# Kernel optimization log

Hardware: AMD Instinct MI355X
Metric: run time of the kernel (lower is better)

The kernel has to match this reference:

```python
import jax, jax.numpy as jnp
import numpy as np

B, V, L = 256, 128000, 2048
EPS = 1e-05


def setup_inputs() -> dict:
    key = jax.random.key(0)
    k1, k2, k3, k4, k5 = jax.random.split(key, 5)
    logits_next = jax.random.normal(k1, (B, V), jnp.float32)
    token_ids = jax.random.randint(k2, (B, L), 0, V, jnp.int32)
    presence_penalties = jax.random.uniform(k3, (B,), jnp.float32) * 1.5
    temperatures = jax.random.uniform(k4, (B,), jnp.float32, 0.5, 1.5)
    # make first quarter of the batch greedy (temperature == 0)
    temperatures = temperatures.at[: B // 4].set(0.0)
    u = jax.random.uniform(k5, (B, V), jnp.float32, 1e-9, 1.0)
    gumbel = -jnp.log(-jnp.log(u))  # Gumbel(0,1) noise for multinomial sampling
    return {
        "logits_next": logits_next,
        "token_ids": token_ids,
        "presence_penalties": presence_penalties,
        "temperatures": temperatures,
        "gumbel": gumbel,
    }


def reference(logits_next, token_ids, presence_penalties, temperatures, gumbel):
    Bn, Vn = logits_next.shape
    # presence mask: 1.0 where token id appeared in the history (counts > 0)
    rows = jnp.arange(Bn, dtype=jnp.int32)[:, None]  # [B,1]
    presence = jnp.zeros((Bn, Vn), logits_next.dtype).at[rows, token_ids].set(1.0)
    penalized = logits_next - presence_penalties[:, None] * presence

    greedy = temperatures < EPS  # [B]
    safe_t = jnp.where(greedy, jnp.float32(1.0), temperatures)
    scaled = penalized / safe_t[:, None]

    # greedy rows: plain argmax; sample rows: Gumbel-max == multinomial(softmax)
    greedy_tok = jnp.argmax(penalized, axis=-1)
    sampled_tok = jnp.argmax(scaled + gumbel, axis=-1)
    token_ids_next = jnp.where(greedy, greedy_tok, sampled_tok)
    return token_ids_next.astype(jnp.int32)
```

## Files before the change

kernel.cpp:

```cpp
#include <hip/hip_runtime.h>
#include <math.h>

#define BATCH 256
#define VOCAB 128000
#define HIST  2048
#define EPS_T 1e-5f

#define MASK_WORDS_ROW (VOCAB / 32)

#define ABLOCK 512

#define SEGS 25
#define SEG_ELEMS (VOCAB / SEGS)
#define SEG_VEC   (SEG_ELEMS / 4)
#define SEG_WORDS (SEG_ELEMS / 32)
#define BBLOCK 256
#define BWAVES (BBLOCK / 64)

__global__ __launch_bounds__(ABLOCK, 1) void mask_kernel(
    const int* __restrict__ token_ids,
    unsigned int* __restrict__ gmask)
{
    __shared__ unsigned int m[MASK_WORDS_ROW];
    const int b = blockIdx.x, tid = threadIdx.x;

    for (int i = tid; i < MASK_WORDS_ROW; i += ABLOCK) m[i] = 0u;
    __syncthreads();

    const int4* rt = (const int4*)(token_ids + (size_t)b * HIST);
    int4 t = rt[tid];
    atomicOr(&m[t.x >> 5], 1u << (t.x & 31));
    atomicOr(&m[t.y >> 5], 1u << (t.y & 31));
    atomicOr(&m[t.z >> 5], 1u << (t.z & 31));
    atomicOr(&m[t.w >> 5], 1u << (t.w & 31));
    __syncthreads();

    unsigned int* gr = gmask + (size_t)b * MASK_WORDS_ROW;
    for (int i = tid; i < MASK_WORDS_ROW; i += ABLOCK) gr[i] = m[i];
}

__device__ __forceinline__ void upd(float s, int idx, float& best, int& besti) {
    if (s > best || (s == best && idx < besti)) { best = s; besti = idx; }
}

__device__ __forceinline__ void body4(float4 l, unsigned w, int sh, float pen,
                                      int idx0, float& best, int& besti) {
    float e[4] = {l.x, l.y, l.z, l.w};
    #pragma unroll
    for (int j = 0; j < 4; j++) {
        float present = (float)((w >> (sh + j)) & 1u);
        float p = e[j] - pen * present;
        upd(p, idx0 + j, best, besti);
    }
}

__device__ __forceinline__ void body4s(float4 l, float4 g, unsigned w, int sh,
                                       float pen, float temp,
                                       int idx0, float& best, int& besti) {
    float e[4]  = {l.x, l.y, l.z, l.w};
    float gv[4] = {g.x, g.y, g.z, g.w};
    #pragma unroll
    for (int j = 0; j < 4; j++) {
        float present = (float)((w >> (sh + j)) & 1u);
        float p = e[j] - pen * present;
        float s = p / temp + gv[j];
        upd(s, idx0 + j, best, besti);
    }
}

__global__ __launch_bounds__(BBLOCK, 1) void scan_kernel(
    const float* __restrict__ logits,
    const float* __restrict__ gumbel,
    const unsigned int* __restrict__ gmask,
    const float* __restrict__ penalties,
    const float* __restrict__ temps,
    float* __restrict__ pvals,
    int*   __restrict__ pidxs)
{
    __shared__ float wval[BWAVES];
    __shared__ int   widx[BWAVES];

    const int blk = blockIdx.x;
    const int b   = blk / SEGS;
    const int seg = blk - b * SEGS;
    const int tid = threadIdx.x;

    const float pen    = penalties[b];
    const float temp   = temps[b];
    const bool  greedy = (temp < EPS_T);

    const float4*       lg = (const float4*)(logits + (size_t)b * VOCAB) + seg * SEG_VEC;
    const float4*       gm = (const float4*)(gumbel + (size_t)b * VOCAB) + seg * SEG_VEC;
    const unsigned int* mw = gmask + (size_t)b * MASK_WORDS_ROW + seg * SEG_WORDS;

    float best  = -INFINITY;
    int   besti = 0x7fffffff;
    const int sh    = (tid * 4) & 31;
    const int abs0  = seg * SEG_ELEMS + tid * 4;
    const int wbase = tid >> 3;

    if (greedy) {
        float4 l0 = lg[tid];
        float4 l1 = lg[tid + 1 * BBLOCK];
        float4 l2 = lg[tid + 2 * BBLOCK];
        float4 l3 = lg[tid + 3 * BBLOCK];
        float4 l4 = lg[tid + 4 * BBLOCK];
        unsigned w0 = mw[wbase];
        unsigned w1 = mw[wbase + 32];
        unsigned w2 = mw[wbase + 64];
        unsigned w3 = mw[wbase + 96];
        unsigned w4 = mw[wbase + 128];
        __builtin_amdgcn_sched_barrier(0);
        body4(l0, w0, sh, pen, abs0 + 0 * BBLOCK * 4, best, besti);
        body4(l1, w1, sh, pen, abs0 + 1 * BBLOCK * 4, best, besti);
        body4(l2, w2, sh, pen, abs0 + 2 * BBLOCK * 4, best, besti);
        body4(l3, w3, sh, pen, abs0 + 3 * BBLOCK * 4, best, besti);
        body4(l4, w4, sh, pen, abs0 + 4 * BBLOCK * 4, best, besti);
    } else {
        float4 l0 = lg[tid];
        float4 l1 = lg[tid + 1 * BBLOCK];
        float4 l2 = lg[tid + 2 * BBLOCK];
        float4 l3 = lg[tid + 3 * BBLOCK];
        float4 l4 = lg[tid + 4 * BBLOCK];
        float4 g0 = gm[tid];
        float4 g1 = gm[tid + 1 * BBLOCK];
        float4 g2 = gm[tid + 2 * BBLOCK];
        float4 g3 = gm[tid + 3 * BBLOCK];
        float4 g4 = gm[tid + 4 * BBLOCK];
        unsigned w0 = mw[wbase];
        unsigned w1 = mw[wbase + 32];
        unsigned w2 = mw[wbase + 64];
        unsigned w3 = mw[wbase + 96];
        unsigned w4 = mw[wbase + 128];
        __builtin_amdgcn_sched_barrier(0);
        body4s(l0, g0, w0, sh, pen, temp, abs0 + 0 * BBLOCK * 4, best, besti);
        body4s(l1, g1, w1, sh, pen, temp, abs0 + 1 * BBLOCK * 4, best, besti);
        body4s(l2, g2, w2, sh, pen, temp, abs0 + 2 * BBLOCK * 4, best, besti);
        body4s(l3, g3, w3, sh, pen, temp, abs0 + 3 * BBLOCK * 4, best, besti);
        body4s(l4, g4, w4, sh, pen, temp, abs0 + 4 * BBLOCK * 4, best, besti);
    }

    #pragma unroll
    for (int off = 32; off > 0; off >>= 1) {
        float ov = __shfl_down(best, off, 64);
        int   oi = __shfl_down(besti, off, 64);
        if (ov > best || (ov == best && oi < besti)) { best = ov; besti = oi; }
    }
    const int wave = tid >> 6, lane = tid & 63;
    if (lane == 0) { wval[wave] = best; widx[wave] = besti; }
    __syncthreads();

    if (tid == 0) {
        #pragma unroll
        for (int wv = 1; wv < BWAVES; wv++) {
            if (wval[wv] > best || (wval[wv] == best && widx[wv] < besti)) {
                best = wval[wv]; besti = widx[wv];
            }
        }
        pvals[seg * BATCH + b] = best;
        pidxs[seg * BATCH + b] = besti;
    }
}

__global__ void reduce_kernel(const float* __restrict__ pvals,
                              const int*   __restrict__ pidxs,
                              int*         __restrict__ out)
{
    const int b = threadIdx.x;
    float best  = pvals[b];
    int   besti = pidxs[b];
    #pragma unroll
    for (int s = 1; s < SEGS; s++) {
        float v = pvals[s * BATCH + b];
        if (v > best) { best = v; besti = pidxs[s * BATCH + b]; }
    }
    out[b] = besti;
}

extern "C" void kernel_launch(void* const* d_in, const int* in_sizes, int n_in,
                              void* d_out, int out_size, void* d_ws, size_t ws_size,
                              hipStream_t stream) {
    const float* logits    = (const float*)d_in[0];
    const int*   token_ids = (const int*)d_in[1];
    const float* penalties = (const float*)d_in[2];
    const float* temps     = (const float*)d_in[3];
    const float* gumbel    = (const float*)d_in[4];
    int* out = (int*)d_out;

    unsigned int* gmask = (unsigned int*)d_ws;
    float* pvals = (float*)((char*)d_ws + (size_t)BATCH * MASK_WORDS_ROW * 4);
    int*   pidxs = (int*)(pvals + SEGS * BATCH);

    mask_kernel<<<BATCH, ABLOCK, 0, stream>>>(token_ids, gmask);
    scan_kernel<<<BATCH * SEGS, BBLOCK, 0, stream>>>(logits, gumbel, gmask,
                                                     penalties, temps, pvals, pidxs);
    reduce_kernel<<<1, BATCH, 0, stream>>>(pvals, pidxs, out);
}
```

Baseline: 270.1 us.

## Fuse presence-mask build into scan and reduce segments via packed 64-bit atomicMax

Drops the separate mask kernel and its global bitmask. Each scan block now reads the row's full token history and builds only its own segment's bitmask in shared memory. The per-segment partial results are folded with a packed key (ordered float bits high, inverted index low) through a 64-bit atomicMax, and a trivial decode kernel unpacks it. This removes a kernel launch and the mask round-trip through global memory. In exchange every block rereads the 8KB history row (25x redundancy per row), adds a memset and two barriers, and pays contention on the global atomics.

```diff
diff --git a/kernel.cpp b/kernel.cpp
--- a/kernel.cpp
+++ b/kernel.cpp
@@ -6,10 +6,6 @@
 #define HIST  2048
 #define EPS_T 1e-5f
 
-#define MASK_WORDS_ROW (VOCAB / 32)
-
-#define ABLOCK 512
-
 #define SEGS 25
 #define SEG_ELEMS (VOCAB / SEGS)
 #define SEG_VEC   (SEG_ELEMS / 4)
@@ -17,26 +13,9 @@
 #define BBLOCK 256
 #define BWAVES (BBLOCK / 64)
 
-__global__ __launch_bounds__(ABLOCK, 1) void mask_kernel(
-    const int* __restrict__ token_ids,
-    unsigned int* __restrict__ gmask)
-{
-    __shared__ unsigned int m[MASK_WORDS_ROW];
-    const int b = blockIdx.x, tid = threadIdx.x;
-
-    for (int i = tid; i < MASK_WORDS_ROW; i += ABLOCK) m[i] = 0u;
-    __syncthreads();
-
-    const int4* rt = (const int4*)(token_ids + (size_t)b * HIST);
-    int4 t = rt[tid];
-    atomicOr(&m[t.x >> 5], 1u << (t.x & 31));
-    atomicOr(&m[t.y >> 5], 1u << (t.y & 31));
-    atomicOr(&m[t.z >> 5], 1u << (t.z & 31));
-    atomicOr(&m[t.w >> 5], 1u << (t.w & 31));
-    __syncthreads();
-
-    unsigned int* gr = gmask + (size_t)b * MASK_WORDS_ROW;
-    for (int i = tid; i < MASK_WORDS_ROW; i += ABLOCK) gr[i] = m[i];
+__device__ __forceinline__ unsigned fkey(float f) {
+    unsigned b = __float_as_uint(f);
+    return (b & 0x80000000u) ? ~b : (b | 0x80000000u);
 }
 
 __device__ __forceinline__ void upd(float s, int idx, float& best, int& besti) {
@@ -68,15 +47,21 @@
     }
 }
 
-__global__ __launch_bounds__(BBLOCK, 1) void scan_kernel(
+__device__ __forceinline__ void setbit(int t, int segBase, unsigned* smask) {
+    unsigned u = (unsigned)(t - segBase);
+    if (u < (unsigned)SEG_ELEMS)
+        atomicOr(&smask[u >> 5], 1u << (u & 31));
+}
+
+__global__ __launch_bounds__(BBLOCK, 1) void fused_scan(
     const float* __restrict__ logits,
     const float* __restrict__ gumbel,
-    const unsigned int* __restrict__ gmask,
+    const int*   __restrict__ token_ids,
     const float* __restrict__ penalties,
     const float* __restrict__ temps,
-    float* __restrict__ pvals,
-    int*   __restrict__ pidxs)
+    unsigned long long* __restrict__ keys)
 {
+    __shared__ unsigned smask[SEG_WORDS];
     __shared__ float wval[BWAVES];
     __shared__ int   widx[BWAVES];
 
@@ -89,14 +74,22 @@
     const float temp   = temps[b];
     const bool  greedy = (temp < EPS_T);
 
-    const float4*       lg = (const float4*)(logits + (size_t)b * VOCAB) + seg * SEG_VEC;
-    const float4*       gm = (const float4*)(gumbel + (size_t)b * VOCAB) + seg * SEG_VEC;
-    const unsigned int* mw = gmask + (size_t)b * MASK_WORDS_ROW + seg * SEG_WORDS;
+    const int segBase = seg * SEG_ELEMS;
+
+    if (tid < SEG_WORDS) smask[tid] = 0u;
+
+    const int4* rt = (const int4*)(token_ids + (size_t)b * HIST);
+    int4 ta = rt[tid];
+    int4 tb = rt[tid + BBLOCK];
+    __builtin_amdgcn_sched_barrier(0);
+
+    const float4* lg = (const float4*)(logits + (size_t)b * VOCAB) + seg * SEG_VEC;
+    const float4* gm = (const float4*)(gumbel + (size_t)b * VOCAB) + seg * SEG_VEC;
 
     float best  = -INFINITY;
     int   besti = 0x7fffffff;
     const int sh    = (tid * 4) & 31;
-    const int abs0  = seg * SEG_ELEMS + tid * 4;
+    const int abs0  = segBase + tid * 4;
     const int wbase = tid >> 3;
 
     if (greedy) {
@@ -105,12 +98,20 @@
         float4 l2 = lg[tid + 2 * BBLOCK];
         float4 l3 = lg[tid + 3 * BBLOCK];
         float4 l4 = lg[tid + 4 * BBLOCK];
-        unsigned w0 = mw[wbase];
-        unsigned w1 = mw[wbase + 32];
-        unsigned w2 = mw[wbase + 64];
-        unsigned w3 = mw[wbase + 96];
-        unsigned w4 = mw[wbase + 128];
         __builtin_amdgcn_sched_barrier(0);
+
+        __syncthreads();
+        setbit(ta.x, segBase, smask); setbit(ta.y, segBase, smask);
+        setbit(ta.z, segBase, smask); setbit(ta.w, segBase, smask);
+        setbit(tb.x, segBase, smask); setbit(tb.y, segBase, smask);
+        setbit(tb.z, segBase, smask); setbit(tb.w, segBase, smask);
+        __syncthreads();
+
+        unsigned w0 = smask[wbase];
+        unsigned w1 = smask[wbase + 32];
+        unsigned w2 = smask[wbase + 64];
+        unsigned w3 = smask[wbase + 96];
+        unsigned w4 = smask[wbase + 128];
         body4(l0, w0, sh, pen, abs0 + 0 * BBLOCK * 4, best, besti);
         body4(l1, w1, sh, pen, abs0 + 1 * BBLOCK * 4, best, besti);
         body4(l2, w2, sh, pen, abs0 + 2 * BBLOCK * 4, best, besti);
@@ -127,12 +128,20 @@
         float4 g2 = gm[tid + 2 * BBLOCK];
         float4 g3 = gm[tid + 3 * BBLOCK];
         float4 g4 = gm[tid + 4 * BBLOCK];
-        unsigned w0 = mw[wbase];
-        unsigned w1 = mw[wbase + 32];
-        unsigned w2 = mw[wbase + 64];
-        unsigned w3 = mw[wbase + 96];
-        unsigned w4 = mw[wbase + 128];
         __builtin_amdgcn_sched_barrier(0);
+
+        __syncthreads();
+        setbit(ta.x, segBase, smask); setbit(ta.y, segBase, smask);
+        setbit(ta.z, segBase, smask); setbit(ta.w, segBase, smask);
+        setbit(tb.x, segBase, smask); setbit(tb.y, segBase, smask);
+        setbit(tb.z, segBase, smask); setbit(tb.w, segBase, smask);
+        __syncthreads();
+
+        unsigned w0 = smask[wbase];
+        unsigned w1 = smask[wbase + 32];
+        unsigned w2 = smask[wbase + 64];
+        unsigned w3 = smask[wbase + 96];
+        unsigned w4 = smask[wbase + 128];
         body4s(l0, g0, w0, sh, pen, temp, abs0 + 0 * BBLOCK * 4, best, besti);
         body4s(l1, g1, w1, sh, pen, temp, abs0 + 1 * BBLOCK * 4, best, besti);
         body4s(l2, g2, w2, sh, pen, temp, abs0 + 2 * BBLOCK * 4, best, besti);
@@ -157,24 +166,17 @@
                 best = wval[wv]; besti = widx[wv];
             }
         }
-        pvals[seg * BATCH + b] = best;
-        pidxs[seg * BATCH + b] = besti;
+        unsigned long long key =
+            ((unsigned long long)fkey(best) << 32) | (unsigned)(~besti);
+        atomicMax(keys + b, key);
     }
 }
 
-__global__ void reduce_kernel(const float* __restrict__ pvals,
-                              const int*   __restrict__ pidxs,
-                              int*         __restrict__ out)
+__global__ void decode_kernel(const unsigned long long* __restrict__ keys,
+                              int* __restrict__ out)
 {
     const int b = threadIdx.x;
-    float best  = pvals[b];
-    int   besti = pidxs[b];
-    #pragma unroll
-    for (int s = 1; s < SEGS; s++) {
-        float v = pvals[s * BATCH + b];
-        if (v > best) { best = v; besti = pidxs[s * BATCH + b]; }
-    }
-    out[b] = besti;
+    out[b] = (int)(~(unsigned)keys[b]);
 }
 
 extern "C" void kernel_launch(void* const* d_in, const int* in_sizes, int n_in,
@@ -187,12 +189,11 @@
     const float* gumbel    = (const float*)d_in[4];
     int* out = (int*)d_out;
 
-    unsigned int* gmask = (unsigned int*)d_ws;
-    float* pvals = (float*)((char*)d_ws + (size_t)BATCH * MASK_WORDS_ROW * 4);
-    int*   pidxs = (int*)(pvals + SEGS * BATCH);
+    unsigned long long* keys = (unsigned long long*)d_ws;
 
-    mask_kernel<<<BATCH, ABLOCK, 0, stream>>>(token_ids, gmask);
-    scan_kernel<<<BATCH * SEGS, BBLOCK, 0, stream>>>(logits, gumbel, gmask,
-                                                     penalties, temps, pvals, pidxs);
-    reduce_kernel<<<1, BATCH, 0, stream>>>(pvals, pidxs, out);
+    hipMemsetAsync(keys, 0, BATCH * sizeof(unsigned long long), stream);
+
+    fused_scan<<<BATCH * SEGS, BBLOCK, 0, stream>>>(logits, gumbel, token_ids,
+                                                    penalties, temps, keys);
+    decode_kernel<<<1, BATCH, 0, stream>>>(keys, out);
 }
```

Result: no change. 268.1 us (-0.7%).
